# Optimization experiments

Hardware: AMD Instinct MI355X
Metric: run time of the kernel (lower is better)

Reference implementation:

```python
import jax, jax.numpy as jnp
import numpy as np

EPS = 1e-5  # torch LayerNorm default

def _std(x):
    # standardize over the last 3 (tensor-feature) modes, biased variance like torch LayerNorm
    mu = jnp.mean(x, axis=(-3, -2, -1), keepdims=True)
    var = jnp.mean(jnp.square(x - mu), axis=(-3, -2, -1), keepdims=True)
    return (x - mu) * jax.lax.rsqrt(var + EPS)

def setup_inputs() -> dict:
    key = jax.random.key(0)
    ks = jax.random.split(key, 12)
    T, B = 512, 16
    a = b = c = 16          # input tensor modes (4096 features)
    ha = hb = hc = 8        # hidden tensor modes (512 features)
    G = 3                   # gates: r, z, n
    f32 = jnp.float32
    return {
        "x": jax.random.normal(ks[0], (T, B, a, b, c), f32),
        "h0": jnp.zeros((B, ha, hb, hc), f32),
        # input-to-hidden TCL3D factors + rank-1 bias + LN affines (stacked over 3 gates)
        "W_fa": jax.random.normal(ks[1], (G, a, ha), f32),
        "W_fb": jax.random.normal(ks[2], (G, b, hb), f32),
        "W_fc": jax.random.normal(ks[3], (G, c, hc), f32),
        "W_ba": jax.random.normal(ks[4], (G, ha), f32),
        "W_bb": jax.random.normal(ks[5], (G, hb), f32),
        "W_bc": jax.random.normal(ks[6], (G, hc), f32),
        "W_lnin_w": jnp.ones((G, a, b, c), f32),
        "W_lnin_b": jnp.zeros((G, a, b, c), f32),
        "W_lnout_w": jnp.ones((G, ha, hb, hc), f32),
        "W_lnout_b": jnp.zeros((G, ha, hb, hc), f32),
        # hidden-to-hidden TCL3D factors + rank-1 bias + LN affines
        "U_fa": jax.random.normal(ks[7], (G, ha, ha), f32),
        "U_fb": jax.random.normal(ks[8], (G, hb, hb), f32),
        "U_fc": jax.random.normal(ks[9], (G, hc, hc), f32),
        "U_ba": jax.random.normal(ks[10], (G, ha), f32),
        "U_bb": jax.random.normal(ks[11], (G, hb), f32),
        "U_bc": jax.random.normal(jax.random.fold_in(key, 99), (G, hc), f32),
        "U_lnin_w": jnp.ones((G, ha, hb, hc), f32),
        "U_lnin_b": jnp.zeros((G, ha, hb, hc), f32),
        "U_lnout_w": jnp.ones((G, ha, hb, hc), f32),
        "U_lnout_b": jnp.zeros((G, ha, hb, hc), f32),
    }

def reference(x, h0, W_fa, W_fb, W_fc, W_ba, W_bb, W_bc,
              W_lnin_w, W_lnin_b, W_lnout_w, W_lnout_b,
              U_fa, U_fb, U_fc, U_ba, U_bb, U_bc,
              U_lnin_w, U_lnin_b, U_lnout_w, U_lnout_b):
    # --- input-to-hidden TCL3D for all 3 gates, batched over time (no h dependence) ---
    xh = _std(x)                                                  # [T,B,a,b,c]
    xg = xh[None] * W_lnin_w[:, None, None] + W_lnin_b[:, None, None]  # [3,T,B,a,b,c]
    Wx = jnp.einsum('gtnabc,gad,gbe,gcf->gtndef', xg, W_fa, W_fb, W_fc)
    Wx = Wx + (W_ba[:, None, None, :, None, None]
               * W_bb[:, None, None, None, :, None]
               * W_bc[:, None, None, None, None, :])              # rank-1 bias
    Wx = _std(Wx) * W_lnout_w[:, None, None] + W_lnout_b[:, None, None]
    Wx = jnp.swapaxes(Wx, 0, 1)                                   # [T,3,B,ha,hb,hc]

    Ub = (U_ba[:, None, :, None, None]
          * U_bb[:, None, None, :, None]
          * U_bc[:, None, None, None, :])                         # [3,1,ha,hb,hc]

    def step(h, wx):
        # hidden-to-hidden TCL3D for all 3 gates
        hh = _std(h)                                              # [B,ha,hb,hc]
        hg = hh[None] * U_lnin_w[:, None] + U_lnin_b[:, None]     # [3,B,ha,hb,hc]
        Uh = jnp.einsum('gndef,gdp,geq,gfr->gnpqr', hg, U_fa, U_fb, U_fc) + Ub
        Uh = _std(Uh) * U_lnout_w[:, None] + U_lnout_b[:, None]
        r = jax.nn.sigmoid(wx[0] + Uh[0])
        z = jax.nn.sigmoid(wx[1] + Uh[1])
        n = jnp.tanh(wx[2] + r * Uh[2])
        h_new = (1.0 - z) * n + z * h
        return h_new, h_new

    _, outs = jax.lax.scan(step, h0, Wx)                          # [T,B,ha,hb,hc]
    return outs
```

## Files before the change

kernel.cpp:

```cpp
#include <hip/hip_runtime.h>

#define EPSV 1e-5f

#define DPP_XADD(v, ctrl)                                                  \
    v += __int_as_float(__builtin_amdgcn_update_dpp(                       \
        0, __float_as_int(v), ctrl, 0xF, 0xF, false))

__device__ __forceinline__ float wave_allsum(float v) {
    DPP_XADD(v, 0x128);
    DPP_XADD(v, 0x124);
    DPP_XADD(v, 0x122);
    DPP_XADD(v, 0x121);
    DPP_XADD(v, 0x142);
    DPP_XADD(v, 0x143);
    return __int_as_float(__builtin_amdgcn_readlane(__float_as_int(v), 63));
}

__device__ __forceinline__ void bar_lds() {
    asm volatile("s_waitcnt lgkmcnt(0)\n\ts_barrier" ::: "memory");
}

__global__ __launch_bounds__(256) void wx_kernel(
    const float* __restrict__ x,
    const float* __restrict__ Wfa, const float* __restrict__ Wfb,
    const float* __restrict__ Wfc,
    const float* __restrict__ Wba, const float* __restrict__ Wbb,
    const float* __restrict__ Wbc,
    const float* __restrict__ lniw, const float* __restrict__ lnib,
    const float* __restrict__ lnow, const float* __restrict__ lnob,
    float* __restrict__ wxo)
{
    __shared__ float Xs[4096];
    __shared__ float S1[2048];
    __shared__ float S2[1024];
    __shared__ float baS[24], bbS[24], bcS[24];
    __shared__ float red[16];

    const int tid  = threadIdx.x;
    const int wid  = tid >> 6, lane = tid & 63;
    const size_t tb = blockIdx.x;
    const float* xp = x + tb * 4096;

    float s = 0.f, s2 = 0.f;
    for (int i = tid; i < 4096; i += 256) {
        float v = xp[i];
        Xs[i] = v;
        s += v; s2 += v * v;
    }
    if (tid < 24) { baS[tid] = Wba[tid]; bbS[tid] = Wbb[tid]; bcS[tid] = Wbc[tid]; }

    __syncthreads();
    #pragma unroll
    for (int off = 32; off > 0; off >>= 1) {
        s  += __shfl_down(s,  off);
        s2 += __shfl_down(s2, off);
    }
    if (lane == 0) { red[wid] = s; red[8 + wid] = s2; }
    __syncthreads();
    s  = red[0] + red[1] + red[2] + red[3];
    s2 = red[8] + red[9] + red[10] + red[11];
    const float muX = s * (1.f / 4096.f);
    const float rsX = rsqrtf(fmaxf(s2 * (1.f / 4096.f) - muX * muX, 0.f) + EPSV);

    const int qh = __builtin_amdgcn_readfirstlane(tid >> 7);
    const int rh = __builtin_amdgcn_readfirstlane(tid >> 6);

    for (int g = 0; g < 3; ++g) {
        {
            float acc[8] = {0,0,0,0,0,0,0,0};
            const int rest = tid;
            const float* lw = lniw + g * 4096;
            const float* lb = lnib + g * 4096;
            #pragma unroll
            for (int m = 0; m < 16; ++m) {
                const float xn = (Xs[m*256 + rest] - muX) * rsX;
                const float xv = fmaf(xn, lw[m*256 + rest], lb[m*256 + rest]);
                #pragma unroll
                for (int p = 0; p < 8; ++p)
                    acc[p] = fmaf(xv, Wfa[(g*16 + m)*8 + p], acc[p]);
            }
            #pragma unroll
            for (int p = 0; p < 8; ++p)
                S1[p*256 + (rest ^ (p << 3))] = acc[p];
        }
        __syncthreads();
        {
            float acc[4] = {0,0,0,0};
            const int rest2 = tid & 127;
            const int c2 = rest2 >> 3, p2 = rest2 & 7;
            #pragma unroll
            for (int m = 0; m < 16; ++m) {
                const float xv = S1[p2*256 + (((m << 4) | c2) ^ (p2 << 3))];
                #pragma unroll
                for (int j = 0; j < 4; ++j)
                    acc[j] = fmaf(xv, Wfb[(g*16 + m)*8 + qh*4 + j], acc[j]);
            }
            #pragma unroll
            for (int j = 0; j < 4; ++j) {
                const int q = qh*4 + j;
                S2[q*128 + (rest2 ^ (q << 3))] = acc[j];
            }
        }
        __syncthreads();
        float v0, v1; int idx0;
        {
            float acc[2] = {0, 0};
            const int rest3 = tid & 63;
            const int q3 = rest3 & 7, pp = rest3 >> 3;
            #pragma unroll
            for (int m = 0; m < 16; ++m) {
                const float xv = S2[q3*128 + (((m << 3) | pp) ^ (q3 << 3))];
                #pragma unroll
                for (int j = 0; j < 2; ++j)
                    acc[j] = fmaf(xv, Wfc[(g*16 + m)*8 + rh*2 + j], acc[j]);
            }
            const float bpq = baS[g*8 + pp] * bbS[g*8 + q3];
            v0 = acc[0] + bpq * bcS[g*8 + rh*2 + 0];
            v1 = acc[1] + bpq * bcS[g*8 + rh*2 + 1];
            idx0 = rest3 * 8 + rh * 2;
        }
        float t = v0 + v1, t2 = v0*v0 + v1*v1;
        __syncthreads();
        #pragma unroll
        for (int off = 32; off > 0; off >>= 1) {
            t  += __shfl_down(t,  off);
            t2 += __shfl_down(t2, off);
        }
        if (lane == 0) { red[wid] = t; red[8 + wid] = t2; }
        __syncthreads();
        t  = red[0] + red[1] + red[2] + red[3];
        t2 = red[8] + red[9] + red[10] + red[11];
        const float mu  = t * (1.f / 512.f);
        const float var = fmaxf(t2 * (1.f / 512.f) - mu * mu, 0.f);
        const float rs  = rsqrtf(var + EPSV);
        float* wp = wxo + (tb * 3 + g) * 512;
        const float2 lw2 = *(const float2*)(lnow + g*512 + idx0);
        const float2 lb2 = *(const float2*)(lnob + g*512 + idx0);
        float2 o2;
        o2.x = fmaf((v0 - mu) * rs, lw2.x, lb2.x);
        o2.y = fmaf((v1 - mu) * rs, lw2.y, lb2.y);
        *(float2*)(wp + idx0) = o2;
    }
}

__global__ __launch_bounds__(192, 1) void scan_kernel(
    const float* __restrict__ wx,
    const float* __restrict__ h0,
    const float* __restrict__ Ufa, const float* __restrict__ Ufb,
    const float* __restrict__ Ufc,
    const float* __restrict__ Uba, const float* __restrict__ Ubb,
    const float* __restrict__ Ubc,
    const float* __restrict__ lniw, const float* __restrict__ lnib,
    const float* __restrict__ lnow, const float* __restrict__ lnob,
    float* __restrict__ out,
    int T, int B)
{
    const int n    = blockIdx.x;
    const int tid  = threadIdx.x;
    const int lane = tid & 63;
    const int gu   = __builtin_amdgcn_readfirstlane(tid >> 6);

    __shared__ float hgS[3][576];
    __shared__ float T1S[3][576];
    __shared__ float T2S[3][576];
    __shared__ float UhS[2][3][576];

    const float* __restrict__ WA = Ufa + gu * 64;
    const float* __restrict__ WB = Ufb + gu * 64;
    const float* __restrict__ WC = Ufc + gu * 64;

    float lnw[8], lnb[8], low8[8], lob8[8], ubias[8];
    {
        const int p_ = lane >> 3, q_ = lane & 7;
        const float bpq = Uba[gu*8 + p_] * Ubb[gu*8 + q_];
        #pragma unroll
        for (int k = 0; k < 8; ++k) {
            lnw[k]   = lniw[gu*512 + lane*8 + k];
            lnb[k]   = lnib[gu*512 + lane*8 + k];
            low8[k]  = lnow[gu*512 + lane*8 + k];
            lob8[k]  = lnob[gu*512 + lane*8 + k];
            ubias[k] = bpq * Ubc[gu*8 + k];
        }
    }

    const int wbase = lane;
    const int rbase = (lane & 7) * 72 + (lane >> 3);

    float hv[8];
    {
        const float4 a = *(const float4*)(h0 + n*512 + lane*8);
        const float4 b = *(const float4*)(h0 + n*512 + lane*8 + 4);
        hv[0]=a.x; hv[1]=a.y; hv[2]=a.z; hv[3]=a.w;
        hv[4]=b.x; hv[5]=b.y; hv[6]=b.z; hv[7]=b.w;
    }

    float uo[8];
    float pfA[3][8], pfB[3][8];

#define LOADWX(TT, PF)                                                     \
    {                                                                      \
        const float* base_ = wx + (((size_t)(TT) * B + n) * 3) * 512       \
                             + lane * 8;                                   \
        _Pragma("unroll")                                                  \
        for (int gg = 0; gg < 3; ++gg) {                                   \
            const float4 A_ = *(const float4*)(base_ + gg*512);            \
            const float4 B_ = *(const float4*)(base_ + gg*512 + 4);        \
            PF[gg][0]=A_.x; PF[gg][1]=A_.y; PF[gg][2]=A_.z; PF[gg][3]=A_.w;\
            PF[gg][4]=B_.x; PF[gg][5]=B_.y; PF[gg][6]=B_.z; PF[gg][7]=B_.w;\
        }                                                                  \
    }

#define WR8(BUFROW, V)                                                     \
    {                                                                      \
        float* p0_ = (BUFROW) + wbase;                                     \
        float* p1_ = p0_ + 288;                                            \
        p0_[0] = V[0]; p0_[72] = V[1]; p0_[144] = V[2]; p0_[216] = V[3];   \
        p1_[0] = V[4]; p1_[72] = V[5]; p1_[144] = V[6]; p1_[216] = V[7];   \
    }

#define RD8(BUFROW, V)                                                     \
    {                                                                      \
        const float* q_ = (BUFROW) + rbase;                                \
        V[0] = q_[0];  V[1] = q_[8];  V[2] = q_[16]; V[3] = q_[24];        \
        V[4] = q_[32]; V[5] = q_[40]; V[6] = q_[48]; V[7] = q_[56];        \
    }

#define RD8W(BUFROW, V)                                                    \
    {                                                                      \
        const float* q0_ = (BUFROW) + wbase;                               \
        const float* q1_ = q0_ + 288;                                      \
        V[0] = q0_[0]; V[1] = q0_[72]; V[2] = q0_[144]; V[3] = q0_[216];   \
        V[4] = q1_[0]; V[5] = q1_[72]; V[6] = q1_[144]; V[7] = q1_[216];   \
    }

#define PIPELINE(PARN)                                                     \
    {                                                                      \
        float sA = 0.f, sB = 0.f;                                          \
        _Pragma("unroll")                                                  \
        for (int k = 0; k < 8; ++k) { sA += hv[k]; sB += hv[k]*hv[k]; }    \
        sA = wave_allsum(sA); sB = wave_allsum(sB);                        \
        const float mu_ = sA * (1.f/512.f);                                \
        const float rs_ = rsqrtf(fmaxf(sB*(1.f/512.f) - mu_*mu_, 0.f)      \
                                 + EPSV);                                  \
        float hg_[8];                                                      \
        _Pragma("unroll")                                                  \
        for (int k = 0; k < 8; ++k)                                        \
            hg_[k] = fmaf((hv[k]-mu_)*rs_, lnw[k], lnb[k]);                \
        WR8(hgS[gu], hg_)                                                  \
        float xv_[8], a_[8];                                               \
        _Pragma("unroll") for (int k = 0; k < 8; ++k) a_[k] = 0.f;         \
        RD8(hgS[gu], xv_)                                                  \
        _Pragma("unroll")                                                  \
        for (int m = 0; m < 8; ++m)                                        \
            _Pragma("unroll")                                              \
            for (int q = 0; q < 8; ++q)                                    \
                a_[q] = fmaf(xv_[m], WA[m*8 + q], a_[q]);                  \
        WR8(T1S[gu], a_)                                                   \
        RD8(T1S[gu], xv_)                                                  \
        _Pragma("unroll") for (int k = 0; k < 8; ++k) a_[k] = 0.f;         \
        _Pragma("unroll")                                                  \
        for (int m = 0; m < 8; ++m)                                        \
            _Pragma("unroll")                                              \
            for (int q = 0; q < 8; ++q)                                    \
                a_[q] = fmaf(xv_[m], WB[m*8 + q], a_[q]);                  \
        WR8(T2S[gu], a_)                                                   \
        RD8(T2S[gu], xv_)                                                  \
        _Pragma("unroll") for (int k = 0; k < 8; ++k) a_[k] = 0.f;         \
        _Pragma("unroll")                                                  \
        for (int m = 0; m < 8; ++m)                                        \
            _Pragma("unroll")                                              \
            for (int q = 0; q < 8; ++q)                                    \
                a_[q] = fmaf(xv_[m], WC[m*8 + q], a_[q]);                  \
        float sC = 0.f, sD = 0.f;                                          \
        _Pragma("unroll")                                                  \
        for (int k = 0; k < 8; ++k) {                                      \
            a_[k] += ubias[k]; sC += a_[k]; sD += a_[k]*a_[k];             \
        }                                                                  \
        sC = wave_allsum(sC); sD = wave_allsum(sD);                        \
        const float mu2_ = sC * (1.f/512.f);                               \
        const float rs2_ = rsqrtf(fmaxf(sD*(1.f/512.f) - mu2_*mu2_, 0.f)   \
                                  + EPSV);                                 \
        _Pragma("unroll")                                                  \
        for (int k = 0; k < 8; ++k)                                        \
            uo[k] = fmaf((a_[k]-mu2_)*rs2_, low8[k], lob8[k]);             \
        WR8(UhS[PARN][gu], uo)                                             \
    }

#define COMBINE(PARC, PF, TT)                                              \
    {                                                                      \
        float ur[8], uz[8], un[8];                                         \
        if (gu == 0) {                                                     \
            _Pragma("unroll")                                              \
            for (int k = 0; k < 8; ++k) ur[k] = uo[k];                     \
            RD8W(UhS[PARC][1], uz)                                         \
            RD8W(UhS[PARC][2], un)                                         \
        } else if (gu == 1) {                                              \
            _Pragma("unroll")                                              \
            for (int k = 0; k < 8; ++k) uz[k] = uo[k];                     \
            RD8W(UhS[PARC][0], ur)                                         \
            RD8W(UhS[PARC][2], un)                                         \
        } else {                                                           \
            _Pragma("unroll")                                              \
            for (int k = 0; k < 8; ++k) un[k] = uo[k];                     \
            RD8W(UhS[PARC][0], ur)                                         \
            RD8W(UhS[PARC][1], uz)                                         \
        }                                                                  \
        _Pragma("unroll")                                                  \
        for (int k = 0; k < 8; ++k) {                                      \
            const float er_ = __expf(-(PF[0][k] + ur[k]));                 \
            const float r_  = __builtin_amdgcn_rcpf(1.f + er_);            \
            const float ez_ = __expf(-(PF[1][k] + uz[k]));                 \
            const float z_  = __builtin_amdgcn_rcpf(1.f + ez_);            \
            const float e2_ = __expf(2.f * (PF[2][k] + r_ * un[k]));       \
            const float nn_ = 1.f - 2.f*__builtin_amdgcn_rcpf(e2_ + 1.f);  \
            hv[k] = (1.f - z_)*nn_ + z_*hv[k];                             \
        }                                                                  \
        if (gu == 0) {                                                     \
            float* op_ = out + ((size_t)(TT) * B + n) * 512 + lane*8;      \
            *(float4*)op_     = make_float4(hv[0], hv[1], hv[2], hv[3]);   \
            *(float4*)(op_+4) = make_float4(hv[4], hv[5], hv[6], hv[7]);   \
        }                                                                  \
    }

    LOADWX(0, pfA);
    PIPELINE(0);

    for (int t = 0; t < T; t += 2) {
        bar_lds();
        if (t + 1 < T) LOADWX(t + 1, pfB);
        COMBINE(0, pfA, t)
        if (t + 1 < T) PIPELINE(1)
        bar_lds();
        if (t + 2 < T) LOADWX(t + 2, pfA);
        COMBINE(1, pfB, t + 1)
        if (t + 2 < T) PIPELINE(0)
    }
#undef LOADWX
#undef WR8
#undef RD8
#undef RD8W
#undef PIPELINE
#undef COMBINE
}

extern "C" void kernel_launch(void* const* d_in, const int* in_sizes, int n_in,
                              void* d_out, int out_size, void* d_ws, size_t ws_size,
                              hipStream_t stream)
{
    const float* x    = (const float*)d_in[0];
    const float* h0   = (const float*)d_in[1];
    const float* Wfa  = (const float*)d_in[2];
    const float* Wfb  = (const float*)d_in[3];
    const float* Wfc  = (const float*)d_in[4];
    const float* Wba  = (const float*)d_in[5];
    const float* Wbb  = (const float*)d_in[6];
    const float* Wbc  = (const float*)d_in[7];
    const float* Wliw = (const float*)d_in[8];
    const float* Wlib = (const float*)d_in[9];
    const float* Wlow = (const float*)d_in[10];
    const float* Wlob = (const float*)d_in[11];
    const float* Ufa  = (const float*)d_in[12];
    const float* Ufb  = (const float*)d_in[13];
    const float* Ufc  = (const float*)d_in[14];
    const float* Uba  = (const float*)d_in[15];
    const float* Ubb  = (const float*)d_in[16];
    const float* Ubc  = (const float*)d_in[17];
    const float* Uliw = (const float*)d_in[18];
    const float* Ulib = (const float*)d_in[19];
    const float* Ulow = (const float*)d_in[20];
    const float* Ulob = (const float*)d_in[21];

    const int B = in_sizes[1] / 512;
    const int T = in_sizes[0] / (B * 4096);

    float* wxws = (float*)d_ws;
    float* out  = (float*)d_out;

    wx_kernel<<<T * B, 256, 0, stream>>>(x, Wfa, Wfb, Wfc, Wba, Wbb, Wbc,
                                         Wliw, Wlib, Wlow, Wlob, wxws);
    scan_kernel<<<B, 192, 0, stream>>>(wxws, h0, Ufa, Ufb, Ufc, Uba, Ubb, Ubc,
                                       Uliw, Ulib, Ulow, Ulob, out, T, B);
}
```

Measured before the change: 915.6 us.

## Hoist recurrent factor weights into registers and single-buffer the Wx prefetch

Loads the three 8x8 per-gate hidden factor matrices once into registers instead of reading them from global memory inside every timestep. The first factor is forced into scalar registers via readfirstlane and the other two into vector registers, using empty asm constraints so the compiler keeps them resident. To make room, the double-buffered Wx prefetch is collapsed into one buffer, and the load is now issued after the combine step rather than before it. This holds 192 extra values in registers and shortens how far ahead the Wx load is issued, so more of its global latency may land on the serial recurrence.

```diff
diff --git a/kernel.cpp b/kernel.cpp
--- a/kernel.cpp
+++ b/kernel.cpp
@@ -1,6 +1,9 @@
 #include <hip/hip_runtime.h>
 
 #define EPSV 1e-5f
+
+#define KEEPV(x) asm volatile("" : "+v"(x))
+#define KEEPS(x) asm volatile("" : "+s"(x))
 
 #define DPP_XADD(v, ctrl)                                                  \
     v += __int_as_float(__builtin_amdgcn_update_dpp(                       \
@@ -165,9 +168,17 @@
     __shared__ float T2S[3][576];
     __shared__ float UhS[2][3][576];
 
-    const float* __restrict__ WA = Ufa + gu * 64;
-    const float* __restrict__ WB = Ufb + gu * 64;
-    const float* __restrict__ WC = Ufc + gu * 64;
+    float wA[64], wB[64], wC[64];
+    #pragma unroll
+    for (int i = 0; i < 64; ++i) {
+        wA[i] = __uint_as_float(__builtin_amdgcn_readfirstlane(
+                    __float_as_uint(Ufa[gu*64 + i])));
+        KEEPS(wA[i]);
+    }
+    #pragma unroll
+    for (int i = 0; i < 64; ++i) { wB[i] = Ufb[gu*64 + i]; KEEPV(wB[i]); }
+    #pragma unroll
+    for (int i = 0; i < 64; ++i) { wC[i] = Ufc[gu*64 + i]; KEEPV(wC[i]); }
 
     float lnw[8], lnb[8], low8[8], lob8[8], ubias[8];
     {
@@ -195,9 +206,9 @@
     }
 
     float uo[8];
-    float pfA[3][8], pfB[3][8];
-
-#define LOADWX(TT, PF)                                                     \
+    float pf[3][8];
+
+#define LOADWX(TT)                                                         \
     {                                                                      \
         const float* base_ = wx + (((size_t)(TT) * B + n) * 3) * 512       \
                              + lane * 8;                                   \
@@ -205,8 +216,8 @@
         for (int gg = 0; gg < 3; ++gg) {                                   \
             const float4 A_ = *(const float4*)(base_ + gg*512);            \
             const float4 B_ = *(const float4*)(base_ + gg*512 + 4);        \
-            PF[gg][0]=A_.x; PF[gg][1]=A_.y; PF[gg][2]=A_.z; PF[gg][3]=A_.w;\
-            PF[gg][4]=B_.x; PF[gg][5]=B_.y; PF[gg][6]=B_.z; PF[gg][7]=B_.w;\
+            pf[gg][0]=A_.x; pf[gg][1]=A_.y; pf[gg][2]=A_.z; pf[gg][3]=A_.w;\
+            pf[gg][4]=B_.x; pf[gg][5]=B_.y; pf[gg][6]=B_.z; pf[gg][7]=B_.w;\
         }                                                                  \
     }
 
@@ -254,7 +265,7 @@
         for (int m = 0; m < 8; ++m)                                        \
             _Pragma("unroll")                                              \
             for (int q = 0; q < 8; ++q)                                    \
-                a_[q] = fmaf(xv_[m], WA[m*8 + q], a_[q]);                  \
+                a_[q] = fmaf(xv_[m], wA[m*8 + q], a_[q]);                  \
         WR8(T1S[gu], a_)                                                   \
         RD8(T1S[gu], xv_)                                                  \
         _Pragma("unroll") for (int k = 0; k < 8; ++k) a_[k] = 0.f;         \
@@ -262,7 +273,7 @@
         for (int m = 0; m < 8; ++m)                                        \
             _Pragma("unroll")                                              \
             for (int q = 0; q < 8; ++q)                                    \
-                a_[q] = fmaf(xv_[m], WB[m*8 + q], a_[q]);                  \
+                a_[q] = fmaf(xv_[m], wB[m*8 + q], a_[q]);                  \
         WR8(T2S[gu], a_)                                                   \
         RD8(T2S[gu], xv_)                                                  \
         _Pragma("unroll") for (int k = 0; k < 8; ++k) a_[k] = 0.f;         \
@@ -270,7 +281,7 @@
         for (int m = 0; m < 8; ++m)                                        \
             _Pragma("unroll")                                              \
             for (int q = 0; q < 8; ++q)                                    \
-                a_[q] = fmaf(xv_[m], WC[m*8 + q], a_[q]);                  \
+                a_[q] = fmaf(xv_[m], wC[m*8 + q], a_[q]);                  \
         float sC = 0.f, sD = 0.f;                                          \
         _Pragma("unroll")                                                  \
         for (int k = 0; k < 8; ++k) {                                      \
@@ -286,7 +297,7 @@
         WR8(UhS[PARN][gu], uo)                                             \
     }
 
-#define COMBINE(PARC, PF, TT)                                              \
+#define COMBINE(PARC, TT)                                                  \
     {                                                                      \
         float ur[8], uz[8], un[8];                                         \
         if (gu == 0) {                                                     \
@@ -307,11 +318,11 @@
         }                                                                  \
         _Pragma("unroll")                                                  \
         for (int k = 0; k < 8; ++k) {                                      \
-            const float er_ = __expf(-(PF[0][k] + ur[k]));                 \
+            const float er_ = __expf(-(pf[0][k] + ur[k]));                 \
             const float r_  = __builtin_amdgcn_rcpf(1.f + er_);            \
-            const float ez_ = __expf(-(PF[1][k] + uz[k]));                 \
+            const float ez_ = __expf(-(pf[1][k] + uz[k]));                 \
             const float z_  = __builtin_amdgcn_rcpf(1.f + ez_);            \
-            const float e2_ = __expf(2.f * (PF[2][k] + r_ * un[k]));       \
+            const float e2_ = __expf(2.f * (pf[2][k] + r_ * un[k]));       \
             const float nn_ = 1.f - 2.f*__builtin_amdgcn_rcpf(e2_ + 1.f);  \
             hv[k] = (1.f - z_)*nn_ + z_*hv[k];                             \
         }                                                                  \
@@ -322,18 +333,22 @@
         }                                                                  \
     }
 
-    LOADWX(0, pfA);
+    LOADWX(0);
     PIPELINE(0);
 
     for (int t = 0; t < T; t += 2) {
         bar_lds();
-        if (t + 1 < T) LOADWX(t + 1, pfB);
-        COMBINE(0, pfA, t)
-        if (t + 1 < T) PIPELINE(1)
+        COMBINE(0, t)
+        if (t + 1 < T) {
+            LOADWX(t + 1);
+            PIPELINE(1)
+        }
         bar_lds();
-        if (t + 2 < T) LOADWX(t + 2, pfA);
-        COMBINE(1, pfB, t + 1)
-        if (t + 2 < T) PIPELINE(0)
+        if (t + 1 < T) COMBINE(1, t + 1)
+        if (t + 2 < T) {
+            LOADWX(t + 2);
+            PIPELINE(0)
+        }
     }
 #undef LOADWX
 #undef WR8
```

Result: faster. 812.2 us (-11.3%).
